# Kernel tuning notes

Measured on AMD Instinct MI355X. Metric: run time of the kernel, lower is better.

The kernel has to match this reference:

```python
import jax, jax.numpy as jnp
import numpy as np

M, N_GRID, DIM = 32, 32, 128
N_SAMPLES = 100000


def setup_inputs() -> dict:
    key = jax.random.key(0)
    k1, k2 = jax.random.split(key)
    x = jax.random.normal(k1, (N_SAMPLES, DIM), dtype=jnp.float32)
    som_weights = jax.random.normal(k2, (M, N_GRID, DIM), dtype=jnp.float32)
    return {"x": x, "som_weights": som_weights}


def reference(x, som_weights):
    # MiniSom.activation_response([v]) puts a 1 at the best-matching unit
    # (argmin Euclidean distance over the m*n prototype grid), then flattens.
    # Batched equivalent: [N, K] squared distances -> argmin -> one-hot.
    K = som_weights.shape[0] * som_weights.shape[1]
    w = som_weights.reshape(K, -1)                       # [K, dim]
    x_sq = jnp.sum(x * x, axis=1, keepdims=True)         # [N, 1]
    w_sq = jnp.sum(w * w, axis=1)                        # [K]
    # squared Euclidean distance; argmin identical to argmin of true distance
    d2 = x_sq + w_sq[None, :] - 2.0 * (x @ w.T)          # [N, K]
    bmu = jnp.argmin(d2, axis=1)                         # [N]
    return jax.nn.one_hot(bmu, K, dtype=jnp.float32)     # [N, K]
```

## Files before the change

kernel.cpp:

```cpp
#include <hip/hip_runtime.h>


typedef __attribute__((ext_vector_type(8))) short bf16x8;
typedef __attribute__((ext_vector_type(4))) float f32x4;

#define SOM_K 1024
#define SOM_D 128
#define MARGIN 0.02f
#define FLAG_CAP 8192

#define WS_WSQ   64
#define WS_W3    8192
#define WS_FLAGS 532480

static __device__ __forceinline__ unsigned short f2bf(float f) {
    unsigned u = __float_as_uint(f);
    return (unsigned short)((u + 0x7FFFu + ((u >> 16) & 1u)) >> 16);
}
static __device__ __forceinline__ float bf2f(unsigned short h) {
    return __uint_as_float(((unsigned)h) << 16);
}

__global__ __launch_bounds__(256) void som_prep(
    const float* __restrict__ w, unsigned short* __restrict__ w3,
    float* __restrict__ wsq, int* __restrict__ flag_count)
{
    __shared__ float ws_[16][SOM_D];
    const int nt = blockIdx.x;
    const int tid = threadIdx.x;

    if (nt == 0 && tid == 0) *flag_count = 0;

    const float* src = w + (size_t)nt * 16 * SOM_D;
    #pragma unroll
    for (int r = 0; r < 8; ++r) {
        const int e = r * 256 + tid;
        ws_[e >> 7][e & 127] = src[e];
    }
    __syncthreads();

    unsigned short* dst = w3 + (size_t)nt * 4096;
    #pragma unroll
    for (int r = 0; r < 2; ++r) {
        const int G = r * 256 + tid;
        const int s = G >> 6;
        const int l = G & 63;
        const int c = l & 15, q = l >> 4;
        bf16x8 v;
        #pragma unroll
        for (int j = 0; j < 8; ++j) {
            const int kk = 32 * s + 8 * q + j;
            const int d = kk & 127;
            const float f = ws_[c][d];
            const unsigned short h = f2bf(f);
            v[j] = (short)((kk & 128) ? f2bf(f - bf2f(h)) : h);
        }
        *(bf16x8*)(dst + G * 8) = v;
    }

    if (tid < 16) {
        double s = 0.0;
        #pragma unroll 16
        for (int d = 0; d < SOM_D; ++d) {
            double v = (double)ws_[tid][d];
            s += v * v;
        }
        wsq[nt * 16 + tid] = (float)s;
    }
}

__global__ __launch_bounds__(256, 3) void som_main(
    const float* __restrict__ x,
    const unsigned short* __restrict__ w3,
    const float* __restrict__ wsq,
    float* __restrict__ out,
    int* __restrict__ flag_count,
    int* __restrict__ flag_list,
    int n_samples)
{
    const int lane = threadIdx.x & 63;
    const int wv   = threadIdx.x >> 6;
    const int c = lane & 15;
    const int q = lane >> 4;
    const int R0 = blockIdx.x * 128 + wv * 32;

    bf16x8 ah[2][4], al[2][4];
    #pragma unroll
    for (int g = 0; g < 2; ++g) {
        int row = R0 + 16 * g + c;
        if (row >= n_samples) row = n_samples - 1;
        const float* xp = x + (size_t)row * SOM_D + 8 * q;
        #pragma unroll
        for (int s = 0; s < 4; ++s) {
            float4 v0 = *(const float4*)(xp + 32 * s);
            float4 v1 = *(const float4*)(xp + 32 * s + 4);
            float xv[8] = {v0.x, v0.y, v0.z, v0.w, v1.x, v1.y, v1.z, v1.w};
            bf16x8 hh, ll;
            #pragma unroll
            for (int j = 0; j < 8; ++j) {
                unsigned short h = f2bf(xv[j]);
                hh[j] = (short)h;
                ll[j] = (short)f2bf(xv[j] - bf2f(h));
            }
            ah[g][s] = hh; al[g][s] = ll;
        }
    }

    float best[2][4], sec[2][4];
    int bk[2][4];
    #pragma unroll
    for (int g = 0; g < 2; ++g)
        #pragma unroll
        for (int r = 0; r < 4; ++r) { best[g][r] = 1e30f; sec[g][r] = 1e30f; bk[g][r] = 0; }

    const unsigned short* wbase = w3 + lane * 8;

    #pragma unroll 1
    for (int nt = 0; nt < 64; ++nt) {
        const int n0 = nt * 16;
        const unsigned short* wp = wbase + (size_t)nt * 4096;
        bf16x8 b[8];
        #pragma unroll
        for (int s = 0; s < 8; ++s) b[s] = *(const bf16x8*)(wp + 512 * s);
        const float wq = wsq[n0 + c];

        f32x4 a0 = {0.f, 0.f, 0.f, 0.f}, a1 = {0.f, 0.f, 0.f, 0.f};
        #pragma unroll
        for (int s = 0; s < 4; ++s) {
            a0 = __builtin_amdgcn_mfma_f32_16x16x32_bf16(ah[0][s], b[s], a0, 0, 0, 0);
            a1 = __builtin_amdgcn_mfma_f32_16x16x32_bf16(ah[1][s], b[s], a1, 0, 0, 0);
        }
        #pragma unroll
        for (int s = 0; s < 4; ++s) {
            a0 = __builtin_amdgcn_mfma_f32_16x16x32_bf16(ah[0][s], b[4 + s], a0, 0, 0, 0);
            a1 = __builtin_amdgcn_mfma_f32_16x16x32_bf16(ah[1][s], b[4 + s], a1, 0, 0, 0);
        }
        #pragma unroll
        for (int s = 0; s < 4; ++s) {
            a0 = __builtin_amdgcn_mfma_f32_16x16x32_bf16(al[0][s], b[s], a0, 0, 0, 0);
            a1 = __builtin_amdgcn_mfma_f32_16x16x32_bf16(al[1][s], b[s], a1, 0, 0, 0);
        }

        #pragma unroll
        for (int r = 0; r < 4; ++r) {
            float s0 = wq - 2.f * a0[r];
            if (s0 < best[0][r]) { sec[0][r] = best[0][r]; best[0][r] = s0; bk[0][r] = n0 + c; }
            else if (s0 < sec[0][r]) sec[0][r] = s0;
            float s1 = wq - 2.f * a1[r];
            if (s1 < best[1][r]) { sec[1][r] = best[1][r]; best[1][r] = s1; bk[1][r] = n0 + c; }
            else if (s1 < sec[1][r]) sec[1][r] = s1;
        }
    }

    #pragma unroll
    for (int g = 0; g < 2; ++g) {
        #pragma unroll
        for (int r = 0; r < 4; ++r) {
            float b0v = best[g][r], s0v = sec[g][r];
            int k0 = bk[g][r];
            #pragma unroll
            for (int m = 1; m < 16; m <<= 1) {
                float ob = __shfl_xor(b0v, m);
                float os = __shfl_xor(s0v, m);
                int   ok = __shfl_xor(k0, m);
                if (ob < b0v || (ob == b0v && ok < k0)) {
                    s0v = fminf(b0v, os); b0v = ob; k0 = ok;
                } else {
                    s0v = fminf(s0v, ob);
                }
            }
            best[g][r] = b0v; sec[g][r] = s0v; bk[g][r] = k0;
        }
    }

    if (c == 0) {
        #pragma unroll
        for (int g = 0; g < 2; ++g) {
            #pragma unroll
            for (int r = 0; r < 4; ++r) {
                const int row = R0 + g * 16 + 4 * q + r;
                if (row < n_samples && (sec[g][r] - best[g][r]) < MARGIN) {
                    int i = atomicAdd(flag_count, 1);
                    if (i < FLAG_CAP) flag_list[i] = row;
                }
            }
        }
    }

    #pragma unroll 1
    for (int rr = 0; rr < 32; ++rr) {
        const int row = R0 + rr;
        if (row >= n_samples) break;
        const int g = rr >> 4, qq = (rr >> 2) & 3, r = rr & 3;
        const int b = __shfl(bk[g][r], qq << 4);
        f32x4* op = (f32x4*)(out + (size_t)row * SOM_K);
        #pragma unroll
        for (int j = 0; j < 4; ++j) {
            const int e = j * 64 + lane;
            f32x4 v = {0.f, 0.f, 0.f, 0.f};
            if ((b >> 2) == e) v[b & 3] = 1.0f;
            op[e] = v;
        }
    }
}

__global__ __launch_bounds__(1024) void som_pass2(
    const float* __restrict__ x,
    const float* __restrict__ w,
    float* __restrict__ out,
    const int* __restrict__ flag_count,
    const int* __restrict__ flag_list)
{
    __shared__ float xs[SOM_D];
    __shared__ double rbest[16];
    __shared__ int    rk[16];

    const int tid  = threadIdx.x;
    const int lane = tid & 63;
    const int wv   = tid >> 6;
    int cnt = *flag_count;
    if (cnt > FLAG_CAP) cnt = FLAG_CAP;

    for (int i = blockIdx.x; i < cnt; i += gridDim.x) {
        const int row = flag_list[i];
        __syncthreads();
        if (tid < SOM_D) xs[tid] = x[(size_t)row * SOM_D + tid];
        __syncthreads();

        const float* wk = w + (size_t)tid * SOM_D;
        double s0 = 0.0, s1 = 0.0;
        #pragma unroll
        for (int d = 0; d < SOM_D; d += 4) {
            float4 wv4 = *(const float4*)(wk + d);
            double w0 = (double)wv4.x, w1 = (double)wv4.y;
            double w2 = (double)wv4.z, w3 = (double)wv4.w;
            s0 += w0 * (w0 - 2.0 * (double)xs[d])     + w2 * (w2 - 2.0 * (double)xs[d + 2]);
            s1 += w1 * (w1 - 2.0 * (double)xs[d + 1]) + w3 * (w3 - 2.0 * (double)xs[d + 3]);
        }
        double sc = s0 + s1;
        int bk = tid;

        #pragma unroll
        for (int off = 32; off > 0; off >>= 1) {
            double os = __shfl_down(sc, off);
            int    ok = __shfl_down(bk, off);
            if (os < sc || (os == sc && ok < bk)) { sc = os; bk = ok; }
        }
        if (lane == 0) { rbest[wv] = sc; rk[wv] = bk; }
        __syncthreads();

        if (tid == 0) {
            double b = rbest[0]; int k0 = rk[0];
            #pragma unroll
            for (int v = 1; v < 16; ++v) {
                if (rbest[v] < b || (rbest[v] == b && rk[v] < k0)) { b = rbest[v]; k0 = rk[v]; }
            }
            rk[0] = k0;
        }
        __syncthreads();
        const int bmu = rk[0];

        out[(size_t)row * SOM_K + tid] = (tid == bmu) ? 1.0f : 0.0f;
    }
}

extern "C" void kernel_launch(void* const* d_in, const int* in_sizes, int n_in,
                              void* d_out, int out_size, void* d_ws, size_t ws_size,
                              hipStream_t stream) {
    const float* x = (const float*)d_in[0];
    const float* w = (const float*)d_in[1];
    float* out = (float*)d_out;

    const int n_samples = in_sizes[0] / SOM_D;

    char* ws = (char*)d_ws;
    int*            flag_count = (int*)ws;
    float*          wsq        = (float*)(ws + WS_WSQ);
    unsigned short* w3         = (unsigned short*)(ws + WS_W3);
    int*            flag_list  = (int*)(ws + WS_FLAGS);

    som_prep<<<64, 256, 0, stream>>>(w, w3, wsq, flag_count);
    const int grid = (n_samples + 127) / 128;
    som_main<<<grid, 256, 0, stream>>>(x, w3, wsq, out, flag_count, flag_list,
                                       n_samples);
    som_pass2<<<256, 1024, 0, stream>>>(x, w, out, flag_count, flag_list);
}
```

Measured before the change: 689.2 us.

## Shrink per-wave rows to 16 and split MFMA accumulators for shorter chains

Each wave now handles 16 sample rows instead of 32, which halves the per-thread register state and doubles the grid size. The launch-bounds occupancy hint is removed. The hi and lo MFMA products go into two independent accumulators that are summed at the end, breaking the single long dependent chain. In exchange, every B fragment is reused by half as many MFMAs, so global or L2 traffic for the weights per sample doubles.

```diff
diff --git a/kernel.cpp b/kernel.cpp
--- a/kernel.cpp
+++ b/kernel.cpp
@@ -69,7 +69,7 @@
     }
 }
 
-__global__ __launch_bounds__(256, 3) void som_main(
+__global__ __launch_bounds__(256) void som_main(
     const float* __restrict__ x,
     const unsigned short* __restrict__ w3,
     const float* __restrict__ wsq,
@@ -82,12 +82,11 @@
     const int wv   = threadIdx.x >> 6;
     const int c = lane & 15;
     const int q = lane >> 4;
-    const int R0 = blockIdx.x * 128 + wv * 32;
-
-    bf16x8 ah[2][4], al[2][4];
-    #pragma unroll
-    for (int g = 0; g < 2; ++g) {
-        int row = R0 + 16 * g + c;
+    const int R0 = blockIdx.x * 64 + wv * 16;
+
+    bf16x8 ah[4], al[4];
+    {
+        int row = R0 + c;
         if (row >= n_samples) row = n_samples - 1;
         const float* xp = x + (size_t)row * SOM_D + 8 * q;
         #pragma unroll
@@ -102,16 +101,14 @@
                 hh[j] = (short)h;
                 ll[j] = (short)f2bf(xv[j] - bf2f(h));
             }
-            ah[g][s] = hh; al[g][s] = ll;
-        }
-    }
-
-    float best[2][4], sec[2][4];
-    int bk[2][4];
-    #pragma unroll
-    for (int g = 0; g < 2; ++g)
-        #pragma unroll
-        for (int r = 0; r < 4; ++r) { best[g][r] = 1e30f; sec[g][r] = 1e30f; bk[g][r] = 0; }
+            ah[s] = hh; al[s] = ll;
+        }
+    }
+
+    float best[4], sec[4];
+    int bk[4];
+    #pragma unroll
+    for (int r = 0; r < 4; ++r) { best[r] = 1e30f; sec[r] = 1e30f; bk[r] = 0; }
 
     const unsigned short* wbase = w3 + lane * 8;
 
@@ -124,75 +121,59 @@
         for (int s = 0; s < 8; ++s) b[s] = *(const bf16x8*)(wp + 512 * s);
         const float wq = wsq[n0 + c];
 
-        f32x4 a0 = {0.f, 0.f, 0.f, 0.f}, a1 = {0.f, 0.f, 0.f, 0.f};
-        #pragma unroll
-        for (int s = 0; s < 4; ++s) {
-            a0 = __builtin_amdgcn_mfma_f32_16x16x32_bf16(ah[0][s], b[s], a0, 0, 0, 0);
-            a1 = __builtin_amdgcn_mfma_f32_16x16x32_bf16(ah[1][s], b[s], a1, 0, 0, 0);
-        }
-        #pragma unroll
-        for (int s = 0; s < 4; ++s) {
-            a0 = __builtin_amdgcn_mfma_f32_16x16x32_bf16(ah[0][s], b[4 + s], a0, 0, 0, 0);
-            a1 = __builtin_amdgcn_mfma_f32_16x16x32_bf16(ah[1][s], b[4 + s], a1, 0, 0, 0);
-        }
-        #pragma unroll
-        for (int s = 0; s < 4; ++s) {
-            a0 = __builtin_amdgcn_mfma_f32_16x16x32_bf16(al[0][s], b[s], a0, 0, 0, 0);
-            a1 = __builtin_amdgcn_mfma_f32_16x16x32_bf16(al[1][s], b[s], a1, 0, 0, 0);
-        }
+        f32x4 aA = {0.f, 0.f, 0.f, 0.f}, aB = {0.f, 0.f, 0.f, 0.f};
+        #pragma unroll
+        for (int s = 0; s < 4; ++s)
+            aA = __builtin_amdgcn_mfma_f32_16x16x32_bf16(ah[s], b[s], aA, 0, 0, 0);
+        #pragma unroll
+        for (int s = 0; s < 4; ++s)
+            aA = __builtin_amdgcn_mfma_f32_16x16x32_bf16(ah[s], b[4 + s], aA, 0, 0, 0);
+        #pragma unroll
+        for (int s = 0; s < 4; ++s)
+            aB = __builtin_amdgcn_mfma_f32_16x16x32_bf16(al[s], b[s], aB, 0, 0, 0);
 
         #pragma unroll
         for (int r = 0; r < 4; ++r) {
-            float s0 = wq - 2.f * a0[r];
-            if (s0 < best[0][r]) { sec[0][r] = best[0][r]; best[0][r] = s0; bk[0][r] = n0 + c; }
-            else if (s0 < sec[0][r]) sec[0][r] = s0;
-            float s1 = wq - 2.f * a1[r];
-            if (s1 < best[1][r]) { sec[1][r] = best[1][r]; best[1][r] = s1; bk[1][r] = n0 + c; }
-            else if (s1 < sec[1][r]) sec[1][r] = s1;
-        }
-    }
-
-    #pragma unroll
-    for (int g = 0; g < 2; ++g) {
+            float s0 = wq - 2.f * (aA[r] + aB[r]);
+            if (s0 < best[r]) { sec[r] = best[r]; best[r] = s0; bk[r] = n0 + c; }
+            else if (s0 < sec[r]) sec[r] = s0;
+        }
+    }
+
+    #pragma unroll
+    for (int r = 0; r < 4; ++r) {
+        float b0v = best[r], s0v = sec[r];
+        int k0 = bk[r];
+        #pragma unroll
+        for (int m = 1; m < 16; m <<= 1) {
+            float ob = __shfl_xor(b0v, m);
+            float os = __shfl_xor(s0v, m);
+            int   ok = __shfl_xor(k0, m);
+            if (ob < b0v || (ob == b0v && ok < k0)) {
+                s0v = fminf(b0v, os); b0v = ob; k0 = ok;
+            } else {
+                s0v = fminf(s0v, ob);
+            }
+        }
+        best[r] = b0v; sec[r] = s0v; bk[r] = k0;
+    }
+
+    if (c == 0) {
         #pragma unroll
         for (int r = 0; r < 4; ++r) {
-            float b0v = best[g][r], s0v = sec[g][r];
-            int k0 = bk[g][r];
-            #pragma unroll
-            for (int m = 1; m < 16; m <<= 1) {
-                float ob = __shfl_xor(b0v, m);
-                float os = __shfl_xor(s0v, m);
-                int   ok = __shfl_xor(k0, m);
-                if (ob < b0v || (ob == b0v && ok < k0)) {
-                    s0v = fminf(b0v, os); b0v = ob; k0 = ok;
-                } else {
-                    s0v = fminf(s0v, ob);
-                }
-            }
-            best[g][r] = b0v; sec[g][r] = s0v; bk[g][r] = k0;
-        }
-    }
-
-    if (c == 0) {
-        #pragma unroll
-        for (int g = 0; g < 2; ++g) {
-            #pragma unroll
-            for (int r = 0; r < 4; ++r) {
-                const int row = R0 + g * 16 + 4 * q + r;
-                if (row < n_samples && (sec[g][r] - best[g][r]) < MARGIN) {
-                    int i = atomicAdd(flag_count, 1);
-                    if (i < FLAG_CAP) flag_list[i] = row;
-                }
+            const int row = R0 + 4 * q + r;
+            if (row < n_samples && (sec[r] - best[r]) < MARGIN) {
+                int i = atomicAdd(flag_count, 1);
+                if (i < FLAG_CAP) flag_list[i] = row;
             }
         }
     }
 
     #pragma unroll 1
-    for (int rr = 0; rr < 32; ++rr) {
+    for (int rr = 0; rr < 16; ++rr) {
         const int row = R0 + rr;
         if (row >= n_samples) break;
-        const int g = rr >> 4, qq = (rr >> 2) & 3, r = rr & 3;
-        const int b = __shfl(bk[g][r], qq << 4);
+        const int b = __shfl(bk[rr & 3], (rr >> 2) << 4);
         f32x4* op = (f32x4*)(out + (size_t)row * SOM_K);
         #pragma unroll
         for (int j = 0; j < 4; ++j) {
@@ -280,7 +261,7 @@
     int*            flag_list  = (int*)(ws + WS_FLAGS);
 
     som_prep<<<64, 256, 0, stream>>>(w, w3, wsq, flag_count);
-    const int grid = (n_samples + 127) / 128;
+    const int grid = (n_samples + 63) / 64;
     som_main<<<grid, 256, 0, stream>>>(x, w3, wsq, out, flag_count, flag_list,
                                        n_samples);
     som_pass2<<<256, 1024, 0, stream>>>(x, w, out, flag_count, flag_list);
```

New measurement: 661.4 us. 1.04x faster.
